# Kernel tuning notes

Hardware: AMD Instinct MI355X
Metric: run time of the kernel (lower is better)

Reference implementation:

```python
import jax, jax.numpy as jnp
import numpy as np

B, N, F_IN, D = 4, 2048, 32, 64  # D = output_dim; gat1: heads=4, d=D//2=32; gat2: heads=1, d=D


def _gat(x, adj_norm, Wq, bq, Wk, bk, Wv, bv, heads, d):
    b, n, _ = x.shape
    q = (x @ Wq + bq).reshape(b, n, heads, d)
    k = (x @ Wk + bk).reshape(b, n, heads, d)
    v = (x @ Wv + bv).reshape(b, n, heads, d)
    scores = jnp.einsum('bihd,bjhd->bhij', q, k) / jnp.sqrt(jnp.float32(d))
    mask = jnp.where(adj_norm == 0, jnp.float32(-1e9), jnp.float32(0.0))  # [N,N]
    w = jax.nn.softmax(scores + mask[None, None], axis=-1)
    out = jnp.einsum('bhij,bjhd->bihd', w, v)
    return out.reshape(b, n, heads * d)


def setup_inputs() -> dict:
    key = jax.random.key(0)
    ks = jax.random.split(key, 12)
    s = 0.05
    x = jax.random.normal(ks[0], (B, N, F_IN), dtype=jnp.float32)
    adj = (jax.random.uniform(ks[1], (N, N)) < 0.02).astype(jnp.float32)  # sparse binary graph
    return {
        'x': x, 'adj': adj,
        'Wp': jax.random.normal(ks[2], (F_IN, D)) * s, 'bp': jnp.zeros((D,), jnp.float32),
        'Wq1': jax.random.normal(ks[3], (F_IN, 2 * D)) * s, 'bq1': jnp.zeros((2 * D,), jnp.float32),
        'Wk1': jax.random.normal(ks[4], (F_IN, 2 * D)) * s, 'bk1': jnp.zeros((2 * D,), jnp.float32),
        'Wv1': jax.random.normal(ks[5], (F_IN, 2 * D)) * s, 'bv1': jnp.zeros((2 * D,), jnp.float32),
        'Wq2': jax.random.normal(ks[6], (2 * D, D)) * s, 'bq2': jnp.zeros((D,), jnp.float32),
        'Wk2': jax.random.normal(ks[7], (2 * D, D)) * s, 'bk2': jnp.zeros((D,), jnp.float32),
        'Wv2': jax.random.normal(ks[8], (2 * D, D)) * s, 'bv2': jnp.zeros((D,), jnp.float32),
        'gamma': jnp.ones((D,), jnp.float32), 'beta': jnp.zeros((D,), jnp.float32),
    }


def reference(x, adj, Wp, bp, Wq1, bq1, Wk1, bk1, Wv1, bv1,
              Wq2, bq2, Wk2, bk2, Wv2, bv2, gamma, beta):
    # row-normalized adjacency (normalize_adjacency)
    adj_n = adj / (jnp.sum(adj, axis=1, keepdims=True) + 1e-6)
    proj = x @ Wp + bp                                   # [B,N,D]
    h = _gat(x, adj_n, Wq1, bq1, Wk1, bk1, Wv1, bv1, 4, D // 2)   # [B,N,2D]
    h = jax.nn.relu(h)                                   # dropout inactive (training=False)
    h = _gat(h, adj_n, Wq2, bq2, Wk2, bk2, Wv2, bv2, 1, D)        # [B,N,D]
    y = h + proj
    mu = jnp.mean(y, axis=-1, keepdims=True)
    var = jnp.var(y, axis=-1, keepdims=True)
    return gamma * (y - mu) / jnp.sqrt(var + 1e-6) + beta
```

## Files before the change

### kernel.cpp

```cpp
#include <hip/hip_runtime.h>
#include <hip/hip_bf16.h>
#include <hip/hip_fp16.h>

#define BB 4
#define NN 2048
#define FIN 32
#define DD 64
#define MAXDEG 128

__device__ __forceinline__ __half2 u2h2(unsigned u) {
    union { unsigned u; __half2 h; } x; x.u = u; return x.h;
}

__global__ __launch_bounds__(128) void csr_gemm1(const float* __restrict__ adj,
    int* __restrict__ deg, int* __restrict__ col,
    const float* __restrict__ x,
    const float* __restrict__ Wp, const float* __restrict__ bp,
    const float* __restrict__ Wq, const float* __restrict__ bq,
    const float* __restrict__ Wk, const float* __restrict__ bk,
    const float* __restrict__ Wv, const float* __restrict__ bv,
    float* __restrict__ proj, __half* __restrict__ q1,
    __half* __restrict__ k1, __half* __restrict__ v1) {
    const int bid = blockIdx.x;
    const int tid = threadIdx.x;

    if (bid < NN / 2) {
        const int lane = tid & 63;
        const int i = bid * 2 + (tid >> 6);
        const unsigned long long below = (1ull << lane) - 1ull;
        int base = 0;
        for (int j0 = 0; j0 < NN; j0 += 256) {
            const float4 a = *(const float4*)(adj + (size_t)i * NN + j0 + lane * 4);
            const bool n0 = a.x != 0.0f, n1 = a.y != 0.0f, n2 = a.z != 0.0f, n3 = a.w != 0.0f;
            const unsigned long long m0 = __ballot(n0);
            const unsigned long long m1 = __ballot(n1);
            const unsigned long long m2 = __ballot(n2);
            const unsigned long long m3 = __ballot(n3);
            int slot = base + __popcll(m0 & below) + __popcll(m1 & below)
                            + __popcll(m2 & below) + __popcll(m3 & below);
            const int jb = j0 + 4 * lane;
            if (n0) { if (slot < MAXDEG) col[i * MAXDEG + slot] = jb;     ++slot; }
            if (n1) { if (slot < MAXDEG) col[i * MAXDEG + slot] = jb + 1; ++slot; }
            if (n2) { if (slot < MAXDEG) col[i * MAXDEG + slot] = jb + 2; ++slot; }
            if (n3) { if (slot < MAXDEG) col[i * MAXDEG + slot] = jb + 3; ++slot; }
            base += __popcll(m0) + __popcll(m1) + __popcll(m2) + __popcll(m3);
        }
        if (lane == 0) deg[i] = base < MAXDEG ? base : MAXDEG;
        return;
    }

    const int r0 = (bid - NN / 2) * 4;
    __shared__ float xs[FIN * 4];
    {
        const int r = tid >> 5, k = tid & 31;
        xs[k * 4 + r] = x[(size_t)r0 * FIN + tid];
    }
    __syncthreads();

    float aq0 = bq[tid], aq1 = aq0, aq2 = aq0, aq3 = aq0;
    float ak0 = bk[tid], ak1 = ak0, ak2 = ak0, ak3 = ak0;
    float av0 = bv[tid], av1 = av0, av2 = av0, av3 = av0;
    #pragma unroll
    for (int k = 0; k < FIN; ++k) {
        const float wq = Wq[k * 128 + tid];
        const float wk = Wk[k * 128 + tid];
        const float wv = Wv[k * 128 + tid];
        const float4 xv = *(const float4*)&xs[k * 4];
        aq0 = fmaf(xv.x, wq, aq0); aq1 = fmaf(xv.y, wq, aq1);
        aq2 = fmaf(xv.z, wq, aq2); aq3 = fmaf(xv.w, wq, aq3);
        ak0 = fmaf(xv.x, wk, ak0); ak1 = fmaf(xv.y, wk, ak1);
        ak2 = fmaf(xv.z, wk, ak2); ak3 = fmaf(xv.w, wk, ak3);
        av0 = fmaf(xv.x, wv, av0); av1 = fmaf(xv.y, wv, av1);
        av2 = fmaf(xv.z, wv, av2); av3 = fmaf(xv.w, wv, av3);
    }
    q1[(size_t)(r0 + 0) * 128 + tid] = __float2half_rn(aq0);
    q1[(size_t)(r0 + 1) * 128 + tid] = __float2half_rn(aq1);
    q1[(size_t)(r0 + 2) * 128 + tid] = __float2half_rn(aq2);
    q1[(size_t)(r0 + 3) * 128 + tid] = __float2half_rn(aq3);
    k1[(size_t)(r0 + 0) * 128 + tid] = __float2half_rn(ak0);
    k1[(size_t)(r0 + 1) * 128 + tid] = __float2half_rn(ak1);
    k1[(size_t)(r0 + 2) * 128 + tid] = __float2half_rn(ak2);
    k1[(size_t)(r0 + 3) * 128 + tid] = __float2half_rn(ak3);
    v1[(size_t)(r0 + 0) * 128 + tid] = __float2half_rn(av0);
    v1[(size_t)(r0 + 1) * 128 + tid] = __float2half_rn(av1);
    v1[(size_t)(r0 + 2) * 128 + tid] = __float2half_rn(av2);
    v1[(size_t)(r0 + 3) * 128 + tid] = __float2half_rn(av3);

    if (tid < 64) {
        float a0 = bp[tid], a1 = a0, a2 = a0, a3 = a0;
        #pragma unroll
        for (int k = 0; k < FIN; ++k) {
            const float wp = Wp[k * 64 + tid];
            const float4 xv = *(const float4*)&xs[k * 4];
            a0 = fmaf(xv.x, wp, a0); a1 = fmaf(xv.y, wp, a1);
            a2 = fmaf(xv.z, wp, a2); a3 = fmaf(xv.w, wp, a3);
        }
        proj[(size_t)(r0 + 0) * 64 + tid] = a0; proj[(size_t)(r0 + 1) * 64 + tid] = a1;
        proj[(size_t)(r0 + 2) * 64 + tid] = a2; proj[(size_t)(r0 + 3) * 64 + tid] = a3;
    }
}

__global__ __launch_bounds__(192) void gemm2_fused(const __half* __restrict__ h,
    const float* __restrict__ Wq, const float* __restrict__ bq,
    const float* __restrict__ Wk, const float* __restrict__ bk,
    const float* __restrict__ Wv, const float* __restrict__ bv,
    __half* __restrict__ q2, __half* __restrict__ k2, __half* __restrict__ v2) {
    const int r0 = blockIdx.x * 8;
    const int tid = threadIdx.x;
    const int mat = tid / 64;
    const int c = tid & 63;
    __shared__ float xs[128][8];
    for (int idx = tid; idx < 512; idx += 192) {
        const __half2 hv = ((const __half2*)(h + (size_t)r0 * 128))[idx];
        const int flat = idx * 2;
        const int r = flat >> 7, k = flat & 127;
        xs[k][r] = __low2float(hv); xs[k + 1][r] = __high2float(hv);
    }
    __syncthreads();

    const float* __restrict__ W   = mat == 0 ? Wq : (mat == 1 ? Wk : Wv);
    const float* __restrict__ bia = mat == 0 ? bq : (mat == 1 ? bk : bv);
    __half* __restrict__ Y        = mat == 0 ? q2 : (mat == 1 ? k2 : v2);

    float acc[8];
    const float b0 = bia[c];
    #pragma unroll
    for (int r = 0; r < 8; ++r) acc[r] = b0;
    #pragma unroll 4
    for (int k = 0; k < 128; ++k) {
        const float w = W[(size_t)k * 64 + c];
        const float4 xa = *(const float4*)&xs[k][0];
        const float4 xb = *(const float4*)&xs[k][4];
        acc[0] = fmaf(xa.x, w, acc[0]); acc[1] = fmaf(xa.y, w, acc[1]);
        acc[2] = fmaf(xa.z, w, acc[2]); acc[3] = fmaf(xa.w, w, acc[3]);
        acc[4] = fmaf(xb.x, w, acc[4]); acc[5] = fmaf(xb.y, w, acc[5]);
        acc[6] = fmaf(xb.z, w, acc[6]); acc[7] = fmaf(xb.w, w, acc[7]);
    }
    #pragma unroll
    for (int r = 0; r < 8; ++r) Y[(size_t)(r0 + r) * 64 + c] = __float2half_rn(acc[r]);
}

__device__ __forceinline__ void map_bi4(int bid, int wid, int& b, int& i) {
    const int xcd = bid & 7;
    b = xcd & 3;
    i = ((xcd >> 2) << 10) | ((bid >> 3) << 2) | wid;
}

__global__ __launch_bounds__(256) void attn1_relu(const __half* __restrict__ q1,
                                                  const __half* __restrict__ k1,
                                                  const __half* __restrict__ v1,
                                                  const int* __restrict__ deg,
                                                  const int* __restrict__ col,
                                                  __half* __restrict__ h) {
    const int wid = threadIdx.x >> 6;
    const int lane = threadIdx.x & 63;
    int b, i;
    map_bi4(blockIdx.x, wid, b, i);

    __shared__ float wsA[4][4][MAXDEG + 8];
    const size_t stride = (size_t)NN * 128;
    const int d = deg[i];
    const int hh = lane >> 4;
    const int t  = lane & 15;

    const uint4* qp4 = (const uint4*)(q1 + (size_t)b * stride + (size_t)i * 128 + hh * 32);
    __half2 qh2[16];
    {
        const uint4 qa = qp4[0], qb = qp4[1], qc = qp4[2], qd = qp4[3];
        qh2[0]  = u2h2(qa.x); qh2[1]  = u2h2(qa.y); qh2[2]  = u2h2(qa.z); qh2[3]  = u2h2(qa.w);
        qh2[4]  = u2h2(qb.x); qh2[5]  = u2h2(qb.y); qh2[6]  = u2h2(qb.z); qh2[7]  = u2h2(qb.w);
        qh2[8]  = u2h2(qc.x); qh2[9]  = u2h2(qc.y); qh2[10] = u2h2(qc.z); qh2[11] = u2h2(qc.w);
        qh2[12] = u2h2(qd.x); qh2[13] = u2h2(qd.y); qh2[14] = u2h2(qd.z); qh2[15] = u2h2(qd.w);
    }

    const float scale = 0.17677669529663687f;
    const int nr = (d + 15) >> 4;
    float sc[8];
    for (int r = 0; r < nr; ++r) {
        const int idx = r * 16 + t;
        float s = -INFINITY;
        if (idx < d) {
            const int j = col[i * MAXDEG + idx];
            const uint4* kr4 = (const uint4*)(k1 + (size_t)b * stride + (size_t)j * 128 + hh * 32);
            __half2 a2 = __float2half2_rn(0.0f), b2 = __float2half2_rn(0.0f);
            #pragma unroll
            for (int w = 0; w < 4; ++w) {
                const uint4 kw = kr4[w];
                a2 = __hfma2(qh2[w * 4 + 0], u2h2(kw.x), a2);
                b2 = __hfma2(qh2[w * 4 + 1], u2h2(kw.y), b2);
                a2 = __hfma2(qh2[w * 4 + 2], u2h2(kw.z), a2);
                b2 = __hfma2(qh2[w * 4 + 3], u2h2(kw.w), b2);
            }
            s = ((__low2float(a2) + __high2float(a2)) +
                 (__low2float(b2) + __high2float(b2))) * scale;
        }
        sc[r] = s;
    }

    float mx = sc[0];
    for (int r = 1; r < nr; ++r) mx = fmaxf(mx, sc[r]);
    #pragma unroll
    for (int off = 8; off >= 1; off >>= 1) mx = fmaxf(mx, __shfl_xor(mx, off));
    float se = 0.0f;
    for (int r = 0; r < nr; ++r) {
        const float e = __expf(sc[r] - mx);
        sc[r] = e;
        se += e;
    }
    #pragma unroll
    for (int off = 8; off >= 1; off >>= 1) se += __shfl_xor(se, off);
    const float inv = (d > 0) ? 1.0f / se : 0.0f;
    for (int r = 0; r < nr; ++r) {
        const int idx = r * 16 + t;
        if (idx < d) wsA[wid][hh][idx] = sc[r] * inv;
    }
    asm volatile("s_waitcnt lgkmcnt(0)" ::: "memory");

    const float* __restrict__ wp = wsA[wid][lane >> 4];
    const int4* __restrict__ cp4 = (const int4*)(col + i * MAXDEG);
    const __half* __restrict__ vrow = v1 + (size_t)b * stride + 2 * lane;
    float a0 = 0.0f, a1 = 0.0f, b0 = 0.0f, b1 = 0.0f;
    float c0 = 0.0f, c1 = 0.0f, e0 = 0.0f, e1 = 0.0f;
    int t2 = 0;
    for (; t2 + 4 <= d; t2 += 4) {
        const int4 j4 = cp4[t2 >> 2];
        const float w0 = wp[t2], w1 = wp[t2 + 1], w2 = wp[t2 + 2], w3 = wp[t2 + 3];
        const __half2 v0 = u2h2(*(const unsigned*)(vrow + (size_t)j4.x * 128));
        const __half2 v1h = u2h2(*(const unsigned*)(vrow + (size_t)j4.y * 128));
        const __half2 v2h = u2h2(*(const unsigned*)(vrow + (size_t)j4.z * 128));
        const __half2 v3h = u2h2(*(const unsigned*)(vrow + (size_t)j4.w * 128));
        a0 = fmaf(w0, __low2float(v0), a0);  a1 = fmaf(w0, __high2float(v0), a1);
        b0 = fmaf(w1, __low2float(v1h), b0); b1 = fmaf(w1, __high2float(v1h), b1);
        c0 = fmaf(w2, __low2float(v2h), c0); c1 = fmaf(w2, __high2float(v2h), c1);
        e0 = fmaf(w3, __low2float(v3h), e0); e1 = fmaf(w3, __high2float(v3h), e1);
    }
    for (; t2 < d; ++t2) {
        const int j = col[i * MAXDEG + t2];
        const float w0 = wp[t2];
        const __half2 v0 = u2h2(*(const unsigned*)(vrow + (size_t)j * 128));
        a0 = fmaf(w0, __low2float(v0), a0);  a1 = fmaf(w0, __high2float(v0), a1);
    }
    float o0 = (a0 + b0) + (c0 + e0);
    float o1 = (a1 + b1) + (c1 + e1);
    if (d == 0) {
        float s0 = 0.0f, s1 = 0.0f;
        for (int j = 0; j < NN; ++j) {
            const __half2 vj = u2h2(*(const unsigned*)(vrow + (size_t)j * 128));
            s0 += __low2float(vj); s1 += __high2float(vj);
        }
        o0 = s0 * (1.0f / NN); o1 = s1 * (1.0f / NN);
    }
    o0 = fmaxf(o0, 0.0f); o1 = fmaxf(o1, 0.0f);
    ((__half2*)(h + (size_t)b * stride + (size_t)i * 128))[lane] =
        __halves2half2(__float2half_rn(o0), __float2half_rn(o1));
}

__global__ __launch_bounds__(256) void attn2_ln(const __half* __restrict__ q2,
                                                const __half* __restrict__ k2,
                                                const __half* __restrict__ v2,
                                                const float* __restrict__ proj,
                                                const int* __restrict__ deg,
                                                const int* __restrict__ col,
                                                const float* __restrict__ gamma,
                                                const float* __restrict__ beta,
                                                float* __restrict__ out) {
    const int wid = threadIdx.x >> 6;
    const int lane = threadIdx.x & 63;
    int b, i;
    map_bi4(blockIdx.x, wid, b, i);

    __shared__ float ws2[4][MAXDEG];
    __shared__ float att_lds[4][64];
    const size_t stride = (size_t)NN * 64;
    const int d = deg[i];

    __half2 qh2[32];
    {
        const uint4* qp4 = (const uint4*)(q2 + (size_t)b * stride + (size_t)i * 64);
        #pragma unroll
        for (int w = 0; w < 8; ++w) {
            const uint4 qw = qp4[w];
            qh2[w * 4 + 0] = u2h2(qw.x); qh2[w * 4 + 1] = u2h2(qw.y);
            qh2[w * 4 + 2] = u2h2(qw.z); qh2[w * 4 + 3] = u2h2(qw.w);
        }
    }

    const float scale = 0.125f;
    const int nr = (d + 63) >> 6;
    float sc[2];
    for (int r = 0; r < nr; ++r) {
        const int idx = r * 64 + lane;
        float s = -INFINITY;
        if (idx < d) {
            const int j = col[i * MAXDEG + idx];
            const uint4* kr4 = (const uint4*)(k2 + (size_t)b * stride + (size_t)j * 64);
            __half2 a2 = __float2half2_rn(0.0f), b2 = __float2half2_rn(0.0f);
            #pragma unroll
            for (int w = 0; w < 8; ++w) {
                const uint4 kw = kr4[w];
                a2 = __hfma2(qh2[w * 4 + 0], u2h2(kw.x), a2);
                b2 = __hfma2(qh2[w * 4 + 1], u2h2(kw.y), b2);
                a2 = __hfma2(qh2[w * 4 + 2], u2h2(kw.z), a2);
                b2 = __hfma2(qh2[w * 4 + 3], u2h2(kw.w), b2);
            }
            s = ((__low2float(a2) + __high2float(a2)) +
                 (__low2float(b2) + __high2float(b2))) * scale;
        }
        sc[r] = s;
    }

    float mx = sc[0];
    for (int r = 1; r < nr; ++r) mx = fmaxf(mx, sc[r]);
    #pragma unroll
    for (int off = 32; off >= 1; off >>= 1) mx = fmaxf(mx, __shfl_xor(mx, off));
    float se = 0.0f;
    for (int r = 0; r < nr; ++r) {
        const float e = __expf(sc[r] - mx);
        sc[r] = e;
        se += e;
    }
    #pragma unroll
    for (int off = 32; off >= 1; off >>= 1) se += __shfl_xor(se, off);
    const float inv = (d > 0) ? 1.0f / se : 0.0f;
    for (int r = 0; r < nr; ++r) {
        const int idx = r * 64 + lane;
        if (idx < d) ws2[wid][idx] = sc[r] * inv;
    }
    asm volatile("s_waitcnt lgkmcnt(0)" ::: "memory");

    const int p = lane & 31, g = lane >> 5;
    const float* __restrict__ wp = ws2[wid];
    const __half* __restrict__ vrow = v2 + (size_t)b * stride + 2 * p;
    float a0 = 0.0f, a1 = 0.0f, b0 = 0.0f, b1 = 0.0f;
    int t2 = g;
    for (; t2 + 2 < d; t2 += 4) {
        const int ja = col[i * MAXDEG + t2], jb = col[i * MAXDEG + t2 + 2];
        const __half2 va = u2h2(*(const unsigned*)(vrow + (size_t)ja * 64));
        const __half2 vb = u2h2(*(const unsigned*)(vrow + (size_t)jb * 64));
        const float wa = wp[t2], wb = wp[t2 + 2];
        a0 = fmaf(wa, __low2float(va), a0); a1 = fmaf(wa, __high2float(va), a1);
        b0 = fmaf(wb, __low2float(vb), b0); b1 = fmaf(wb, __high2float(vb), b1);
    }
    if (t2 < d) {
        const int ja = col[i * MAXDEG + t2];
        const __half2 va = u2h2(*(const unsigned*)(vrow + (size_t)ja * 64));
        const float wa = wp[t2];
        a0 = fmaf(wa, __low2float(va), a0); a1 = fmaf(wa, __high2float(va), a1);
    }
    a0 += b0; a1 += b1;
    a0 += __shfl_xor(a0, 32);
    a1 += __shfl_xor(a1, 32);
    if (g == 0) { att_lds[wid][2 * p] = a0; att_lds[wid][2 * p + 1] = a1; }
    asm volatile("s_waitcnt lgkmcnt(0)" ::: "memory");
    float att = att_lds[wid][lane];
    if (d == 0) {
        float a = 0.0f;
        const __half* vr = v2 + (size_t)b * stride + lane;
        for (int j = 0; j < NN; ++j) a += __half2float(vr[(size_t)j * 64]);
        att = a * (1.0f / NN);
    }

    const float y = att + proj[(size_t)b * stride + (size_t)i * 64 + lane];
    float s = y;
    s += __shfl_xor(s, 32); s += __shfl_xor(s, 16); s += __shfl_xor(s, 8);
    s += __shfl_xor(s, 4);  s += __shfl_xor(s, 2);  s += __shfl_xor(s, 1);
    const float mu = s * (1.0f / 64.0f);
    const float yc = y - mu;
    float sq = yc * yc;
    sq += __shfl_xor(sq, 32); sq += __shfl_xor(sq, 16); sq += __shfl_xor(sq, 8);
    sq += __shfl_xor(sq, 4);  sq += __shfl_xor(sq, 2);  sq += __shfl_xor(sq, 1);
    const float var = sq * (1.0f / 64.0f);
    out[(size_t)b * stride + (size_t)i * 64 + lane] =
        gamma[lane] * yc * rsqrtf(var + 1e-6f) + beta[lane];
}

extern "C" void kernel_launch(void* const* d_in, const int* in_sizes, int n_in,
                              void* d_out, int out_size, void* d_ws, size_t ws_size,
                              hipStream_t stream) {
    const float* x     = (const float*)d_in[0];
    const float* adj   = (const float*)d_in[1];
    const float* Wp    = (const float*)d_in[2];
    const float* bp    = (const float*)d_in[3];
    const float* Wq1   = (const float*)d_in[4];
    const float* bq1   = (const float*)d_in[5];
    const float* Wk1   = (const float*)d_in[6];
    const float* bk1   = (const float*)d_in[7];
    const float* Wv1   = (const float*)d_in[8];
    const float* bv1   = (const float*)d_in[9];
    const float* Wq2   = (const float*)d_in[10];
    const float* bq2   = (const float*)d_in[11];
    const float* Wk2   = (const float*)d_in[12];
    const float* bk2   = (const float*)d_in[13];
    const float* Wv2   = (const float*)d_in[14];
    const float* bv2   = (const float*)d_in[15];
    const float* gamma = (const float*)d_in[16];
    const float* beta  = (const float*)d_in[17];
    float* out = (float*)d_out;

    char* ws = (char*)d_ws;
    size_t off = 0;
    auto alloc = [&](size_t bytes) {
        void* p = ws + off;
        off = (off + bytes + 255) & ~(size_t)255;
        return p;
    };
    int*    deg  = (int*)   alloc((size_t)NN * 4);
    int*    col  = (int*)   alloc((size_t)NN * MAXDEG * 4);
    float*  proj = (float*) alloc((size_t)BB * NN * 64 * 4);
    __half* q1   = (__half*)alloc((size_t)BB * NN * 128 * 2);
    __half* k1   = (__half*)alloc((size_t)BB * NN * 128 * 2);
    __half* v1   = (__half*)alloc((size_t)BB * NN * 128 * 2);
    __half* h    = (__half*)alloc((size_t)BB * NN * 128 * 2);
    __half* q2   = (__half*)alloc((size_t)BB * NN * 64 * 2);
    __half* k2   = (__half*)alloc((size_t)BB * NN * 64 * 2);
    __half* v2   = (__half*)alloc((size_t)BB * NN * 64 * 2);

    csr_gemm1<<<NN / 2 + BB * NN / 4, 128, 0, stream>>>(
        adj, deg, col, x, Wp, bp, Wq1, bq1, Wk1, bk1, Wv1, bv1, proj, q1, k1, v1);

    attn1_relu<<<BB * NN / 4, 256, 0, stream>>>(q1, k1, v1, deg, col, h);

    gemm2_fused<<<BB * NN / 8, 192, 0, stream>>>(h, Wq2, bq2, Wk2, bk2, Wv2, bv2,
                                                 q2, k2, v2);

    attn2_ln<<<BB * NN / 4, 256, 0, stream>>>(q2, k2, v2, proj, deg, col, gamma, beta, out);
}
```

Before: 66.81 us.

## Remap GEMM blocks per XCD and prewarm K/V/col lines in attention kernels

Result: slower. 68.24 us (+2.1%).

```diff
diff --git a/kernel.cpp b/kernel.cpp
--- a/kernel.cpp
+++ b/kernel.cpp
@@ -11,6 +11,7 @@
 __device__ __forceinline__ __half2 u2h2(unsigned u) {
     union { unsigned u; __half2 h; } x; x.u = u; return x.h;
 }
+
 
 __global__ __launch_bounds__(128) void csr_gemm1(const float* __restrict__ adj,
     int* __restrict__ deg, int* __restrict__ col,
@@ -49,7 +50,11 @@
         return;
     }
 
-    const int r0 = (bid - NN / 2) * 4;
+    const int g = bid - NN / 2;
+    const int b = g & 3;
+    const int half = (g >> 2) & 1;
+    const int w = g >> 3;
+    const int r0 = b * NN + half * 1024 + w * 4;
     __shared__ float xs[FIN * 4];
     {
         const int r = tid >> 5, k = tid & 31;
@@ -105,7 +110,11 @@
     const float* __restrict__ Wk, const float* __restrict__ bk,
     const float* __restrict__ Wv, const float* __restrict__ bv,
     __half* __restrict__ q2, __half* __restrict__ k2, __half* __restrict__ v2) {
-    const int r0 = blockIdx.x * 8;
+    const int bid = blockIdx.x;
+    const int b = bid & 3;
+    const int half = (bid >> 2) & 1;
+    const int w = bid >> 3;
+    const int r0 = b * NN + half * 1024 + w * 8;
     const int tid = threadIdx.x;
     const int mat = tid / 64;
     const int c = tid & 63;
@@ -128,13 +137,13 @@
     for (int r = 0; r < 8; ++r) acc[r] = b0;
     #pragma unroll 4
     for (int k = 0; k < 128; ++k) {
-        const float w = W[(size_t)k * 64 + c];
+        const float wv = W[(size_t)k * 64 + c];
         const float4 xa = *(const float4*)&xs[k][0];
         const float4 xb = *(const float4*)&xs[k][4];
-        acc[0] = fmaf(xa.x, w, acc[0]); acc[1] = fmaf(xa.y, w, acc[1]);
-        acc[2] = fmaf(xa.z, w, acc[2]); acc[3] = fmaf(xa.w, w, acc[3]);
-        acc[4] = fmaf(xb.x, w, acc[4]); acc[5] = fmaf(xb.y, w, acc[5]);
-        acc[6] = fmaf(xb.z, w, acc[6]); acc[7] = fmaf(xb.w, w, acc[7]);
+        acc[0] = fmaf(xa.x, wv, acc[0]); acc[1] = fmaf(xa.y, wv, acc[1]);
+        acc[2] = fmaf(xa.z, wv, acc[2]); acc[3] = fmaf(xa.w, wv, acc[3]);
+        acc[4] = fmaf(xb.x, wv, acc[4]); acc[5] = fmaf(xb.y, wv, acc[5]);
+        acc[6] = fmaf(xb.z, wv, acc[6]); acc[7] = fmaf(xb.w, wv, acc[7]);
     }
     #pragma unroll
     for (int r = 0; r < 8; ++r) Y[(size_t)(r0 + r) * 64 + c] = __float2half_rn(acc[r]);
@@ -157,8 +166,24 @@
     int b, i;
     map_bi4(blockIdx.x, wid, b, i);
 
-    __shared__ float wsA[4][4][MAXDEG + 8];
     const size_t stride = (size_t)NN * 128;
+
+    const int rank = blockIdx.x >> 3;
+    unsigned keep = 0u;
+    {
+        const int tid = threadIdx.x;
+        const uint4* kw4 = (const uint4*)(k1 + (size_t)b * stride) + (size_t)rank * 128;
+        const uint4* vw4 = (const uint4*)(v1 + (size_t)b * stride) + (size_t)rank * 128;
+        const int i0 = (((blockIdx.x & 7) >> 2) << 10) | (rank << 2);
+        const uint4* cw4 = (const uint4*)(col + (size_t)i0 * MAXDEG);
+        uint4 wa, wb;
+        if (tid < 128) { wa = kw4[tid]; wb = cw4[tid]; }
+        else           { wa = vw4[tid - 128];
+                         wb = (tid < 192) ? ((const uint4*)(q1 + (size_t)b * stride + (size_t)i0 * 128))[tid - 128]
+                                          : make_uint4(0, 0, 0, 0); }
+        keep = wa.x ^ wa.y ^ wa.z ^ wa.w ^ wb.x ^ wb.y ^ wb.z ^ wb.w;
+    }
+
     const int d = deg[i];
     const int hh = lane >> 4;
     const int t  = lane & 15;
@@ -172,6 +197,8 @@
         qh2[8]  = u2h2(qc.x); qh2[9]  = u2h2(qc.y); qh2[10] = u2h2(qc.z); qh2[11] = u2h2(qc.w);
         qh2[12] = u2h2(qd.x); qh2[13] = u2h2(qd.y); qh2[14] = u2h2(qd.z); qh2[15] = u2h2(qd.w);
     }
+
+    __shared__ float wsA[4][4][MAXDEG + 8];
 
     const float scale = 0.17677669529663687f;
     const int nr = (d + 15) >> 4;
@@ -253,6 +280,7 @@
     o0 = fmaxf(o0, 0.0f); o1 = fmaxf(o1, 0.0f);
     ((__half2*)(h + (size_t)b * stride + (size_t)i * 128))[lane] =
         __halves2half2(__float2half_rn(o0), __float2half_rn(o1));
+    asm volatile("" :: "v"(keep));
 }
 
 __global__ __launch_bounds__(256) void attn2_ln(const __half* __restrict__ q2,
@@ -269,9 +297,25 @@
     int b, i;
     map_bi4(blockIdx.x, wid, b, i);
 
+    const size_t stride = (size_t)NN * 64;
+
+    const int rank = blockIdx.x >> 3;
+    unsigned keep = 0u;
+    {
+        const int tid = threadIdx.x;
+        const uint4* kw4 = (const uint4*)(k2 + (size_t)b * stride) + (size_t)rank * 64;
+        const uint4* vw4 = (const uint4*)(v2 + (size_t)b * stride) + (size_t)rank * 64;
+        const int i0 = (((blockIdx.x & 7) >> 2) << 10) | (rank << 2);
+        const uint4* pw4 = (const uint4*)(proj + (size_t)b * stride + (size_t)i0 * 64);
+        uint4 wa = make_uint4(0, 0, 0, 0);
+        if (tid < 64)        wa = kw4[tid];
+        else if (tid < 128)  wa = vw4[tid - 64];
+        else if (tid < 192)  wa = pw4[tid - 128];
+        keep = wa.x ^ wa.y ^ wa.z ^ wa.w;
+    }
+
     __shared__ float ws2[4][MAXDEG];
     __shared__ float att_lds[4][64];
-    const size_t stride = (size_t)NN * 64;
     const int d = deg[i];
 
     __half2 qh2[32];
@@ -372,6 +416,7 @@
     const float var = sq * (1.0f / 64.0f);
     out[(size_t)b * stride + (size_t)i * 64 + lane] =
         gamma[lane] * yc * rsqrtf(var + 1e-6f) + beta[lane];
+    asm volatile("" :: "v"(keep));
 }
 
 extern "C" void kernel_launch(void* const* d_in, const int* in_sizes, int n_in,
```

## Split attention dot products across lanes and remap GEMM blocks to XCD order

Applied to the files above, without the earlier changes.

After: 64.51 us. -3.4%, faster.

```diff
diff --git a/kernel.cpp b/kernel.cpp
--- a/kernel.cpp
+++ b/kernel.cpp
@@ -49,7 +49,11 @@
         return;
     }
 
-    const int r0 = (bid - NN / 2) * 4;
+    const int g = bid - NN / 2;
+    const int b = g & 3;
+    const int half = (g >> 2) & 1;
+    const int w = g >> 3;
+    const int r0 = b * NN + half * 1024 + w * 4;
     __shared__ float xs[FIN * 4];
     {
         const int r = tid >> 5, k = tid & 31;
@@ -105,7 +109,11 @@
     const float* __restrict__ Wk, const float* __restrict__ bk,
     const float* __restrict__ Wv, const float* __restrict__ bv,
     __half* __restrict__ q2, __half* __restrict__ k2, __half* __restrict__ v2) {
-    const int r0 = blockIdx.x * 8;
+    const int bid = blockIdx.x;
+    const int b = bid & 3;
+    const int half = (bid >> 2) & 1;
+    const int w = bid >> 3;
+    const int r0 = b * NN + half * 1024 + w * 8;
     const int tid = threadIdx.x;
     const int mat = tid / 64;
     const int c = tid & 63;
@@ -128,13 +136,13 @@
     for (int r = 0; r < 8; ++r) acc[r] = b0;
     #pragma unroll 4
     for (int k = 0; k < 128; ++k) {
-        const float w = W[(size_t)k * 64 + c];
+        const float wv = W[(size_t)k * 64 + c];
         const float4 xa = *(const float4*)&xs[k][0];
         const float4 xb = *(const float4*)&xs[k][4];
-        acc[0] = fmaf(xa.x, w, acc[0]); acc[1] = fmaf(xa.y, w, acc[1]);
-        acc[2] = fmaf(xa.z, w, acc[2]); acc[3] = fmaf(xa.w, w, acc[3]);
-        acc[4] = fmaf(xb.x, w, acc[4]); acc[5] = fmaf(xb.y, w, acc[5]);
-        acc[6] = fmaf(xb.z, w, acc[6]); acc[7] = fmaf(xb.w, w, acc[7]);
+        acc[0] = fmaf(xa.x, wv, acc[0]); acc[1] = fmaf(xa.y, wv, acc[1]);
+        acc[2] = fmaf(xa.z, wv, acc[2]); acc[3] = fmaf(xa.w, wv, acc[3]);
+        acc[4] = fmaf(xb.x, wv, acc[4]); acc[5] = fmaf(xb.y, wv, acc[5]);
+        acc[6] = fmaf(xb.z, wv, acc[6]); acc[7] = fmaf(xb.w, wv, acc[7]);
     }
     #pragma unroll
     for (int r = 0; r < 8; ++r) Y[(size_t)(r0 + r) * 64 + c] = __float2half_rn(acc[r]);
@@ -159,66 +167,76 @@
 
     __shared__ float wsA[4][4][MAXDEG + 8];
     const size_t stride = (size_t)NN * 128;
+    const size_t bbase = (size_t)b * stride;
     const int d = deg[i];
-    const int hh = lane >> 4;
-    const int t  = lane & 15;
-
-    const uint4* qp4 = (const uint4*)(q1 + (size_t)b * stride + (size_t)i * 128 + hh * 32);
-    __half2 qh2[16];
+
+    int jA = 0, jB = 0;
+    if (lane < d) jA = col[i * MAXDEG + lane];
+    if (64 + lane < d) jB = col[i * MAXDEG + 64 + lane];
+
+    const int hh   = lane >> 4;
+    const int t    = lane & 15;
+    const int nbr8 = t & 7;
+    const int e    = t >> 3;
+
+    __half2 qh[8];
     {
-        const uint4 qa = qp4[0], qb = qp4[1], qc = qp4[2], qd = qp4[3];
-        qh2[0]  = u2h2(qa.x); qh2[1]  = u2h2(qa.y); qh2[2]  = u2h2(qa.z); qh2[3]  = u2h2(qa.w);
-        qh2[4]  = u2h2(qb.x); qh2[5]  = u2h2(qb.y); qh2[6]  = u2h2(qb.z); qh2[7]  = u2h2(qb.w);
-        qh2[8]  = u2h2(qc.x); qh2[9]  = u2h2(qc.y); qh2[10] = u2h2(qc.z); qh2[11] = u2h2(qc.w);
-        qh2[12] = u2h2(qd.x); qh2[13] = u2h2(qd.y); qh2[14] = u2h2(qd.z); qh2[15] = u2h2(qd.w);
+        const __half* qbase = q1 + bbase + (size_t)i * 128 + hh * 32 + e * 16;
+        const uint4 qa = *(const uint4*)qbase;
+        const uint4 qb = *(const uint4*)(qbase + 8);
+        qh[0] = u2h2(qa.x); qh[1] = u2h2(qa.y); qh[2] = u2h2(qa.z); qh[3] = u2h2(qa.w);
+        qh[4] = u2h2(qb.x); qh[5] = u2h2(qb.y); qh[6] = u2h2(qb.z); qh[7] = u2h2(qb.w);
     }
 
     const float scale = 0.17677669529663687f;
-    const int nr = (d + 15) >> 4;
-    float sc[8];
+    const int nr = (d + 7) >> 3;
+    float sc[16];
     for (int r = 0; r < nr; ++r) {
-        const int idx = r * 16 + t;
-        float s = -INFINITY;
-        if (idx < d) {
-            const int j = col[i * MAXDEG + idx];
-            const uint4* kr4 = (const uint4*)(k1 + (size_t)b * stride + (size_t)j * 128 + hh * 32);
+        const int slot = r * 8 + nbr8;
+        const int jx = __shfl(jA, slot & 63);
+        const int jy = __shfl(jB, slot & 63);
+        const int j = (slot < 64) ? jx : jy;
+        float p = 0.0f;
+        if (slot < d) {
+            const __half* kr = k1 + bbase + (size_t)j * 128 + hh * 32 + e * 16;
+            const uint4 ka = *(const uint4*)kr;
+            const uint4 kb = *(const uint4*)(kr + 8);
             __half2 a2 = __float2half2_rn(0.0f), b2 = __float2half2_rn(0.0f);
-            #pragma unroll
-            for (int w = 0; w < 4; ++w) {
-                const uint4 kw = kr4[w];
-                a2 = __hfma2(qh2[w * 4 + 0], u2h2(kw.x), a2);
-                b2 = __hfma2(qh2[w * 4 + 1], u2h2(kw.y), b2);
-                a2 = __hfma2(qh2[w * 4 + 2], u2h2(kw.z), a2);
-                b2 = __hfma2(qh2[w * 4 + 3], u2h2(kw.w), b2);
-            }
-            s = ((__low2float(a2) + __high2float(a2)) +
-                 (__low2float(b2) + __high2float(b2))) * scale;
-        }
-        sc[r] = s;
-    }
-
-    float mx = sc[0];
+            a2 = __hfma2(qh[0], u2h2(ka.x), a2); b2 = __hfma2(qh[1], u2h2(ka.y), b2);
+            a2 = __hfma2(qh[2], u2h2(ka.z), a2); b2 = __hfma2(qh[3], u2h2(ka.w), b2);
+            a2 = __hfma2(qh[4], u2h2(kb.x), a2); b2 = __hfma2(qh[5], u2h2(kb.y), b2);
+            a2 = __hfma2(qh[6], u2h2(kb.z), a2); b2 = __hfma2(qh[7], u2h2(kb.w), b2);
+            p = (__low2float(a2) + __high2float(a2)) +
+                (__low2float(b2) + __high2float(b2));
+        }
+        p += __shfl_xor(p, 8);
+        sc[r] = (slot < d) ? p * scale : -INFINITY;
+    }
+
+    float mx = (nr > 0) ? sc[0] : -INFINITY;
     for (int r = 1; r < nr; ++r) mx = fmaxf(mx, sc[r]);
     #pragma unroll
     for (int off = 8; off >= 1; off >>= 1) mx = fmaxf(mx, __shfl_xor(mx, off));
     float se = 0.0f;
     for (int r = 0; r < nr; ++r) {
-        const float e = __expf(sc[r] - mx);
-        sc[r] = e;
-        se += e;
+        const float ex = __expf(sc[r] - mx);
+        sc[r] = ex;
+        se += ex;
     }
     #pragma unroll
     for (int off = 8; off >= 1; off >>= 1) se += __shfl_xor(se, off);
-    const float inv = (d > 0) ? 1.0f / se : 0.0f;
-    for (int r = 0; r < nr; ++r) {
-        const int idx = r * 16 + t;
-        if (idx < d) wsA[wid][hh][idx] = sc[r] * inv;
+    const float inv = (d > 0) ? 2.0f / se : 0.0f;
+    if (e == 0) {
+        for (int r = 0; r < nr; ++r) {
+            const int slot = r * 8 + nbr8;
+            if (slot < d) wsA[wid][hh][slot] = sc[r] * inv;
+        }
     }
     asm volatile("s_waitcnt lgkmcnt(0)" ::: "memory");
 
     const float* __restrict__ wp = wsA[wid][lane >> 4];
     const int4* __restrict__ cp4 = (const int4*)(col + i * MAXDEG);
-    const __half* __restrict__ vrow = v1 + (size_t)b * stride + 2 * lane;
+    const __half* __restrict__ vrow = v1 + bbase + 2 * lane;
     float a0 = 0.0f, a1 = 0.0f, b0 = 0.0f, b1 = 0.0f;
     float c0 = 0.0f, c1 = 0.0f, e0 = 0.0f, e1 = 0.0f;
     int t2 = 0;
@@ -251,7 +269,7 @@
         o0 = s0 * (1.0f / NN); o1 = s1 * (1.0f / NN);
     }
     o0 = fmaxf(o0, 0.0f); o1 = fmaxf(o1, 0.0f);
-    ((__half2*)(h + (size_t)b * stride + (size_t)i * 128))[lane] =
+    ((__half2*)(h + bbase + (size_t)i * 128))[lane] =
         __halves2half2(__float2half_rn(o0), __float2half_rn(o1));
 }
 
@@ -272,67 +290,71 @@
     __shared__ float ws2[4][MAXDEG];
     __shared__ float att_lds[4][64];
     const size_t stride = (size_t)NN * 64;
+    const size_t bbase = (size_t)b * stride;
     const int d = deg[i];
 
-    __half2 qh2[32];
+    int jA = 0, jB = 0;
+    if (lane < d) jA = col[i * MAXDEG + lane];
+    if (64 + lane < d) jB = col[i * MAXDEG + 64 + lane];
+
+    const int g = lane >> 3;
+    const int e = lane & 7;
+
+    __half2 qh[4];
     {
-        const uint4* qp4 = (const uint4*)(q2 + (size_t)b * stride + (size_t)i * 64);
-        #pragma unroll
-        for (int w = 0; w < 8; ++w) {
-            const uint4 qw = qp4[w];
-            qh2[w * 4 + 0] = u2h2(qw.x); qh2[w * 4 + 1] = u2h2(qw.y);
-            qh2[w * 4 + 2] = u2h2(qw.z); qh2[w * 4 + 3] = u2h2(qw.w);
-        }
+        const uint4 qa = *(const uint4*)(q2 + bbase + (size_t)i * 64 + e * 8);
+        qh[0] = u2h2(qa.x); qh[1] = u2h2(qa.y); qh[2] = u2h2(qa.z); qh[3] = u2h2(qa.w);
     }
 
     const float scale = 0.125f;
-    const int nr = (d + 63) >> 6;
-    float sc[2];
+    const int nr = (d + 7) >> 3;
+    float sc[16];
     for (int r = 0; r < nr; ++r) {
-        const int idx = r * 64 + lane;
-        float s = -INFINITY;
-        if (idx < d) {
-            const int j = col[i * MAXDEG + idx];
-            const uint4* kr4 = (const uint4*)(k2 + (size_t)b * stride + (size_t)j * 64);
+        const int slot = r * 8 + g;
+        const int jx = __shfl(jA, slot & 63);
+        const int jy = __shfl(jB, slot & 63);
+        const int j = (slot < 64) ? jx : jy;
+        float p = 0.0f;
+        if (slot < d) {
+            const uint4 ka = *(const uint4*)(k2 + bbase + (size_t)j * 64 + e * 8);
             __half2 a2 = __float2half2_rn(0.0f), b2 = __float2half2_rn(0.0f);
-            #pragma unroll
-            for (int w = 0; w < 8; ++w) {
-                const uint4 kw = kr4[w];
-                a2 = __hfma2(qh2[w * 4 + 0], u2h2(kw.x), a2);
-                b2 = __hfma2(qh2[w * 4 + 1], u2h2(kw.y), b2);
-                a2 = __hfma2(qh2[w * 4 + 2], u2h2(kw.z), a2);
-                b2 = __hfma2(qh2[w * 4 + 3], u2h2(kw.w), b2);
-            }
-            s = ((__low2float(a2) + __high2float(a2)) +
-                 (__low2float(b2) + __high2float(b2))) * scale;
-        }
-        sc[r] = s;
-    }
-
-    float mx = sc[0];
+            a2 = __hfma2(qh[0], u2h2(ka.x), a2); b2 = __hfma2(qh[1], u2h2(ka.y), b2);
+            a2 = __hfma2(qh[2], u2h2(ka.z), a2); b2 = __hfma2(qh[3], u2h2(ka.w), b2);
+            p = (__low2float(a2) + __high2float(a2)) +
+                (__low2float(b2) + __high2float(b2));
+        }
+        p += __shfl_xor(p, 1);
+        p += __shfl_xor(p, 2);
+        p += __shfl_xor(p, 4);
+        sc[r] = (slot < d) ? p * scale : -INFINITY;
+    }
+
+    float mx = (nr > 0) ? sc[0] : -INFINITY;
     for (int r = 1; r < nr; ++r) mx = fmaxf(mx, sc[r]);
     #pragma unroll
     for (int off = 32; off >= 1; off >>= 1) mx = fmaxf(mx, __shfl_xor(mx, off));
     float se = 0.0f;
     for (int r = 0; r < nr; ++r) {
-        const float e = __expf(sc[r] - mx);
-        sc[r] = e;
-        se += e;
+        const float ex = __expf(sc[r] - mx);
+        sc[r] = ex;
+        se += ex;
     }
     #pragma unroll
     for (int off = 32; off >= 1; off >>= 1) se += __shfl_xor(se, off);
-    const float inv = (d > 0) ? 1.0f / se : 0.0f;
-    for (int r = 0; r < nr; ++r) {
-        const int idx = r * 64 + lane;
-        if (idx < d) ws2[wid][idx] = sc[r] * inv;
+    const float inv = (d > 0) ? 8.0f / se : 0.0f;
+    if (e == 0) {
+        for (int r = 0; r < nr; ++r) {
+            const int slot = r * 8 + g;
+            if (slot < d) ws2[wid][slot] = sc[r] * inv;
+        }
     }
     asm volatile("s_waitcnt lgkmcnt(0)" ::: "memory");
 
-    const int p = lane & 31, g = lane >> 5;
+    const int p = lane & 31, g2 = lane >> 5;
     const float* __restrict__ wp = ws2[wid];
-    const __half* __restrict__ vrow = v2 + (size_t)b * stride + 2 * p;
+    const __half* __restrict__ vrow = v2 + bbase + 2 * p;
     float a0 = 0.0f, a1 = 0.0f, b0 = 0.0f, b1 = 0.0f;
-    int t2 = g;
+    int t2 = g2;
     for (; t2 + 2 < d; t2 += 4) {
         const int ja = col[i * MAXDEG + t2], jb = col[i * MAXDEG + t2 + 2];
         const __half2 va = u2h2(*(const unsigned*)(vrow + (size_t)ja * 64));
@@ -350,17 +372,17 @@
     a0 += b0; a1 += b1;
     a0 += __shfl_xor(a0, 32);
     a1 += __shfl_xor(a1, 32);
-    if (g == 0) { att_lds[wid][2 * p] = a0; att_lds[wid][2 * p + 1] = a1; }
+    if (g2 == 0) { att_lds[wid][2 * p] = a0; att_lds[wid][2 * p + 1] = a1; }
     asm volatile("s_waitcnt lgkmcnt(0)" ::: "memory");
     float att = att_lds[wid][lane];
     if (d == 0) {
         float a = 0.0f;
-        const __half* vr = v2 + (size_t)b * stride + lane;
+        const __half* vr = v2 + bbase + lane;
         for (int j = 0; j < NN; ++j) a += __half2float(vr[(size_t)j * 64]);
         att = a * (1.0f / NN);
     }
 
-    const float y = att + proj[(size_t)b * stride + (size_t)i * 64 + lane];
+    const float y = att + proj[bbase + (size_t)i * 64 + lane];
     float s = y;
     s += __shfl_xor(s, 32); s += __shfl_xor(s, 16); s += __shfl_xor(s, 8);
     s += __shfl_xor(s, 4);  s += __shfl_xor(s, 2);  s += __shfl_xor(s, 1);
@@ -370,7 +392,7 @@
     sq += __shfl_xor(sq, 32); sq += __shfl_xor(sq, 16); sq += __shfl_xor(sq, 8);
     sq += __shfl_xor(sq, 4);  sq += __shfl_xor(sq, 2);  sq += __shfl_xor(sq, 1);
     const float var = sq * (1.0f / 64.0f);
-    out[(size_t)b * stride + (size_t)i * 64 + lane] =
+    out[bbase + (size_t)i * 64 + lane] =
         gamma[lane] * yc * rsqrtf(var + 1e-6f) + beta[lane];
 }
 
```
